# Optimization experiments

Hardware: AMD Instinct MI355X
Metric: run time of the kernel (lower is better)

## Reference

```python
import jax, jax.numpy as jnp
import numpy as np

DIM = 512
HEADS = 8
DHEAD = 64
INNER = HEADS * DHEAD
CHUNK = 8
GAMMA = 1.0
EPS = 1e-8
LN_EPS = 1e-5


def setup_inputs() -> dict:
    key = jax.random.key(0)
    ks = jax.random.split(key, 10)
    B, N = 64, 256
    return {
        "q": jax.random.normal(ks[0], (B, N, DIM), jnp.float32),
        "k": jax.random.normal(ks[1], (B, N, DIM), jnp.float32),
        "v": jax.random.normal(ks[2], (B, N, DIM), jnp.float32),
        "ln_gamma": jnp.ones((DIM,), jnp.float32),
        "ln_beta": jnp.zeros((DIM,), jnp.float32),
        "W_in": jax.random.normal(ks[3], (DIM, INNER), jnp.float32) / np.sqrt(DIM),
        "W_out": jax.random.normal(ks[4], (INNER, DIM), jnp.float32) / np.sqrt(INNER),
        "b_out": jnp.zeros((DIM,), jnp.float32),
        "cov_logit": jnp.asarray(0.6, jnp.float32),
        "var_logit": jnp.asarray(0.2, jnp.float32),
        "use_advanced": 1,
    }


def _layernorm(x, g, b):
    mu = jnp.mean(x, axis=-1, keepdims=True)
    var = jnp.mean(jnp.square(x - mu), axis=-1, keepdims=True)
    return (x - mu) * jax.lax.rsqrt(var + LN_EPS) * g + b


def _transform(t, ln_gamma, ln_beta, W_in):
    # [B,N,dim] -> [h,B,N,d]
    B, N, _ = t.shape
    f = _layernorm(t, ln_gamma, ln_beta) @ W_in
    return f.reshape(B, N, HEADS, DHEAD).transpose(2, 0, 1, 3)


def _chunk_stats(E):
    # E: [M, N, d], chunks of size CHUNK over M. Returns per-chunk scalars V, C of shape [M//CHUNK].
    M, N, d = E.shape
    nc = M // CHUNK
    Ec = E.reshape(nc, CHUNK, N, d)
    # variance component: torch.var is unbiased (ddof=1) over seq dim
    sigma = jnp.sqrt(jnp.var(Ec, axis=2, ddof=1) + EPS)  # [nc, CHUNK, d]
    V = jnp.mean(jax.nn.relu(GAMMA - sigma), axis=(1, 2))  # [nc]
    # covariance component: per-sample off-diagonal energy, averaged per chunk
    centered = Ec - jnp.mean(Ec, axis=2, keepdims=True)
    cov = jnp.einsum("csni,csnj->csij", centered, centered) / (N - 1)  # [nc,CHUNK,d,d]
    total = jnp.sum(jnp.square(cov), axis=(2, 3))
    diag = jnp.sum(jnp.square(jnp.diagonal(cov, axis1=2, axis2=3)), axis=2)
    C = jnp.mean((total - diag) / d, axis=1)  # [nc]
    return V, C


def reference(q, k, v, ln_gamma, ln_beta, W_in, W_out, b_out, cov_logit, var_logit, use_advanced):
    f_q = _transform(q, ln_gamma, ln_beta, W_in)  # [h,B,N,d]
    f_k = _transform(k, ln_gamma, ln_beta, W_in)
    f_v = _transform(v, ln_gamma, ln_beta, W_in)
    h, B, N, d = f_q.shape

    # cosine similarity
    dots_qk = jnp.einsum("hbnd,hbmd->hbnm", f_q, f_k)
    qn = jnp.linalg.norm(f_q, axis=-1)  # [h,B,N]
    kn = jnp.linalg.norm(f_k, axis=-1)
    cosine_sim = dots_qk / (qn[..., :, None] * kn[..., None, :])

    if use_advanced:
        Vq, Cq = _chunk_stats(f_q.reshape(h * B, N, d))
        Vk, Ck = _chunk_stats(f_k.reshape(h * B, N, d))
        var_component = jnp.repeat(Vq * Vk, CHUNK).reshape(h, B, 1, 1)
        cov_component = jnp.repeat(Cq * Ck, CHUNK).reshape(h, B, 1, 1)
    else:
        qc = f_q - jnp.mean(f_q, axis=-1, keepdims=True)
        kc = f_k - jnp.mean(f_k, axis=-1, keepdims=True)
        cov_component = jnp.einsum("hbnd,hbmd->hbnm", qc, kc) / d
        q_var = jnp.var(f_q, axis=-1, ddof=1, keepdims=True)  # [h,B,N,1]
        k_var = jnp.var(f_k, axis=-1, ddof=1, keepdims=True)
        var_component = (q_var * jnp.swapaxes(k_var, -1, -2)) / d

    cov_w = jax.nn.sigmoid(cov_logit)
    var_w = jax.nn.sigmoid(var_logit)
    cos_w = 1.0 - cov_w - var_w
    dots = cos_w * cosine_sim + cov_w * cov_component + var_w * var_component
    out = jnp.einsum("hbnm,hbmd->hbnd", dots, f_v)
    out = out.transpose(1, 2, 0, 3).reshape(B, N, h * d)
    return out @ W_out + b_out
```

## Files before the change

### kernel.cpp

```cpp
#include <hip/hip_runtime.h>
#include <cstdint>
#include <cstddef>

#define DIM    512
#define HEADS  8
#define DHEAD  64
#define NSEQ   256
#define BATCH  64
#define NROWS  (BATCH * NSEQ)
#define HB     (HEADS * BATCH)

typedef unsigned short u16;
typedef __bf16 bf16x8 __attribute__((ext_vector_type(8)));
typedef float  f32x4  __attribute__((ext_vector_type(4)));

__device__ __forceinline__ float sigmoidf_(float x) { return 1.0f / (1.0f + expf(-x)); }

__device__ __forceinline__ u16 f2bf(float f) {
    union { float f; unsigned u; } a; a.f = f;
    return (u16)((a.u + 0x7fffu + ((a.u >> 16) & 1u)) >> 16);
}

__device__ __forceinline__ void gload16(const void* g, void* l) {
    __builtin_amdgcn_global_load_lds((const __attribute__((address_space(1))) void*)g,
                                     (__attribute__((address_space(3))) void*)l, 16, 0, 0);
}

__global__ __launch_bounds__(256)
void transpose_cast_kernel(const float* __restrict__ W0, const float* __restrict__ W1,
                           u16* __restrict__ WT)
{
    __shared__ float tile[64][65];
    const int t = threadIdx.x;
    const int bx = blockIdx.x * 64, by = blockIdx.y * 64;
    const float* W = blockIdx.z ? W1 : W0;
    u16* dst = WT + (size_t)blockIdx.z * 512 * 512;
#pragma unroll
    for (int i = 0; i < 16; ++i) {
        int idx = i * 256 + t, r = idx >> 6, c = idx & 63;
        tile[r][c] = W[(size_t)(by + r) * DIM + bx + c];
    }
    __syncthreads();
#pragma unroll
    for (int i = 0; i < 16; ++i) {
        int idx = i * 256 + t, r = idx >> 6, c = idx & 63;
        dst[(size_t)(bx + r) * DIM + by + c] = f2bf(tile[c][r]);
    }
}

__global__ __launch_bounds__(256)
void ln_cast_kernel(const float* __restrict__ qp, const float* __restrict__ kp,
                    const float* __restrict__ vp, const float* __restrict__ gam,
                    const float* __restrict__ bet, u16* __restrict__ out)
{
    const int wid = threadIdx.x >> 6, lane = threadIdx.x & 63;
    const int row = blockIdx.x * 4 + wid;
    const int tns = row >> 14, lr = row & 16383;
    const float* X = (tns == 0) ? qp : (tns == 1) ? kp : vp;
    const float* xr = X + (size_t)lr * DIM;
    float4 a = *(const float4*)(xr + lane * 8);
    float4 b = *(const float4*)(xr + lane * 8 + 4);
    float v[8] = {a.x, a.y, a.z, a.w, b.x, b.y, b.z, b.w};
    float s = 0.f;
#pragma unroll
    for (int i = 0; i < 8; ++i) s += v[i];
#pragma unroll
    for (int o = 32; o > 0; o >>= 1) s += __shfl_xor(s, o, 64);
    const float mu = s * (1.f / DIM);
    float sq = 0.f;
#pragma unroll
    for (int i = 0; i < 8; ++i) { float d = v[i] - mu; sq += d * d; }
#pragma unroll
    for (int o = 32; o > 0; o >>= 1) sq += __shfl_xor(sq, o, 64);
    const float rstd = rsqrtf(sq * (1.f / DIM) + 1e-5f);
    float4 g0 = *(const float4*)(gam + lane * 8), g1 = *(const float4*)(gam + lane * 8 + 4);
    float4 b0 = *(const float4*)(bet + lane * 8), b1 = *(const float4*)(bet + lane * 8 + 4);
    float gv[8] = {g0.x, g0.y, g0.z, g0.w, g1.x, g1.y, g1.z, g1.w};
    float bv[8] = {b0.x, b0.y, b0.z, b0.w, b1.x, b1.y, b1.z, b1.w};
    union { u16 h[8]; uint4 u; } o16;
#pragma unroll
    for (int i = 0; i < 8; ++i) o16.h[i] = f2bf((v[i] - mu) * rstd * gv[i] + bv[i]);
    *(uint4*)(out + (size_t)row * DIM + lane * 8) = o16.u;
}

__global__ __launch_bounds__(256)
void in_gemm_kernel(const u16* __restrict__ A, const u16* __restrict__ BT,
                    u16* __restrict__ FT, u16* __restrict__ Fseq)
{
    __shared__ u16 shm[128 * 136];
    u16* Ct = shm;
    const int t = threadIdx.x, lane = t & 63, w = t >> 6;
    const int wr = w >> 1, wc = w & 1;
    const int flat = blockIdx.y * 4 + blockIdx.x;
    const int rt = (flat & 7) * 48 + ((flat >> 3) >> 2);
    const int c0 = ((flat >> 3) & 3) * 128;
    const int r0 = rt * 128;
    const int cl = lane & 15, q = lane >> 4;

    f32x4 acc[4][4];
#pragma unroll
    for (int i = 0; i < 4; ++i)
#pragma unroll
        for (int j = 0; j < 4; ++j) acc[i][j] = (f32x4){0.f, 0.f, 0.f, 0.f};

#define STAGE_IN(buf, kk)                                                        \
    {                                                                            \
        _Pragma("unroll")                                                        \
        for (int i = 0; i < 2; ++i) {                                            \
            int idx = i * 256 + t;                                               \
            int row = idx >> 2, ch = idx & 3;                                    \
            gload16(A  + (size_t)(r0 + row) * DIM + (kk) + ch * 8,               \
                    shm + (buf) * 4096 + idx * 8);                               \
            gload16(BT + (size_t)(c0 + row) * DIM + (kk) + ch * 8,               \
                    shm + 8192 + (buf) * 4096 + idx * 8);                        \
        }                                                                        \
    }

#define COMPUTE_IN(buf)                                                          \
    {                                                                            \
        const u16* As = shm + (buf) * 4096;                                      \
        const u16* Bs = shm + 8192 + (buf) * 4096;                               \
        bf16x8 af[4], bfr[4];                                                    \
        _Pragma("unroll")                                                        \
        for (int mi = 0; mi < 4; ++mi)                                           \
            af[mi] = *(const bf16x8*)(As + (wr * 64 + mi * 16 + cl) * 32 + q * 8); \
        _Pragma("unroll")                                                        \
        for (int ni = 0; ni < 4; ++ni)                                           \
            bfr[ni] = *(const bf16x8*)(Bs + (wc * 64 + ni * 16 + cl) * 32 + q * 8); \
        _Pragma("unroll")                                                        \
        for (int mi = 0; mi < 4; ++mi)                                           \
            _Pragma("unroll")                                                    \
            for (int ni = 0; ni < 4; ++ni)                                       \
                acc[mi][ni] = __builtin_amdgcn_mfma_f32_16x16x32_bf16(af[mi],    \
                                  bfr[ni], acc[mi][ni], 0, 0, 0);                \
    }

    STAGE_IN(0, 0);
    __syncthreads();
    for (int k0 = 0; k0 < DIM; k0 += 64) {
        STAGE_IN(1, k0 + 32);
        COMPUTE_IN(0);
        __syncthreads();
        if (k0 + 64 < DIM) STAGE_IN(0, k0 + 64);
        COMPUTE_IN(1);
        __syncthreads();
    }
#undef STAGE_IN
#undef COMPUTE_IN

    const int tns = r0 >> 14, b = (r0 >> 8) & 63, n0 = r0 & 255;
    const int lr0 = r0 & 16383;

    if (tns == 0) {
#pragma unroll
        for (int mi = 0; mi < 4; ++mi) {
            int lrow = wr * 64 + mi * 16 + q * 4;
#pragma unroll
            for (int ni = 0; ni < 4; ++ni) {
                int lcol = wc * 64 + ni * 16 + cl;
#pragma unroll
                for (int r = 0; r < 4; ++r)
                    Ct[(lrow + r) * 136 + lcol] = f2bf(acc[mi][ni][r]);
            }
        }
        __syncthreads();
#pragma unroll
        for (int i = 0; i < 8; ++i) {
            int idx = t + 256 * i, row = idx >> 4, ch = idx & 15;
            *(uint4*)(Fseq + (size_t)(lr0 + row) * DIM + c0 + ch * 8) =
                *(const uint4*)(Ct + row * 136 + ch * 8);
        }
        __syncthreads();
    }
#pragma unroll
    for (int mi = 0; mi < 4; ++mi) {
        int lrow = wr * 64 + mi * 16 + q * 4;
#pragma unroll
        for (int ni = 0; ni < 4; ++ni) {
            int lcol = wc * 64 + ni * 16 + cl;
#pragma unroll
            for (int r = 0; r < 4; ++r)
                Ct[lcol * 136 + lrow + r] = f2bf(acc[mi][ni][r]);
        }
    }
    __syncthreads();
#pragma unroll
    for (int i = 0; i < 8; ++i) {
        int idx = t + 256 * i, lc = idx >> 4, ch = idx & 15;
        *(uint4*)(FT + (((size_t)(tns * 64 + b) * 512 + c0 + lc) * 256 + n0 + ch * 8)) =
            *(const uint4*)(Ct + lc * 136 + ch * 8);
    }
}

__global__ __launch_bounds__(256)
void stats_kernel(const u16* __restrict__ FT, float* __restrict__ norms,
                  float2* __restrict__ vc)
{
    __shared__ u16 ET[64 * 264];
    __shared__ float mu[64];
    __shared__ float red[4][64];
    __shared__ float wr3[4][3];
    const int hb = blockIdx.x, tns = blockIdx.y, h = hb >> 6, b = hb & 63;
    const int t = threadIdx.x, lane = t & 63, w = t >> 6, cl = lane & 15, q = lane >> 4;
    const size_t Fb = ((size_t)(tns * 64 + b) * 512 + h * 64) * 256;

#pragma unroll
    for (int i = 0; i < 8; ++i) {
        int idx = t + 256 * i;
        int row = idx >> 5, ch = idx & 31;
        *(bf16x8*)(ET + row * 264 + ch * 8) =
            *(const bf16x8*)(FT + Fb + (size_t)row * 256 + ch * 8);
    }
    __syncthreads();

    {
        float s = 0.f;
#pragma unroll
        for (int d = 0; d < 64; ++d) {
            float x = (float)*(const __bf16*)(ET + d * 264 + t);
            s += x * x;
        }
        norms[((size_t)tns * HB + hb) * 256 + t] = sqrtf(s);
    }
    {
        int d = t & 63, part = t >> 6;
        float s = 0.f;
#pragma unroll
        for (int i = 0; i < 8; ++i) {
            bf16x8 v8 = *(const bf16x8*)(ET + d * 264 + part * 64 + i * 8);
#pragma unroll
            for (int j = 0; j < 8; ++j) s += (float)v8[j];
        }
        red[part][d] = s;
    }
    __syncthreads();
    if (t < 64) mu[t] = (red[0][t] + red[1][t] + red[2][t] + red[3][t]) * (1.f / 256.f);
    __syncthreads();

    f32x4 g[4];
#pragma unroll
    for (int nj = 0; nj < 4; ++nj) g[nj] = (f32x4){0.f, 0.f, 0.f, 0.f};
#pragma unroll
    for (int ks = 0; ks < 8; ++ks) {
        bf16x8 af = *(const bf16x8*)(ET + (16 * w + cl) * 264 + ks * 32 + q * 8);
#pragma unroll
        for (int nj = 0; nj < 4; ++nj) {
            bf16x8 bfr = *(const bf16x8*)(ET + (16 * nj + cl) * 264 + ks * 32 + q * 8);
            g[nj] = __builtin_amdgcn_mfma_f32_16x16x32_bf16(af, bfr, g[nj], 0, 0, 0);
        }
    }
    float t2 = 0.f, d2 = 0.f, vs = 0.f;
#pragma unroll
    for (int nj = 0; nj < 4; ++nj) {
        int j = 16 * nj + cl;
        float mj = mu[j];
#pragma unroll
        for (int r = 0; r < 4; ++r) {
            int i = 16 * w + 4 * q + r;
            float gc = (g[nj][r] - 256.f * mu[i] * mj) * (1.f / 255.f);
            float g2 = gc * gc;
            t2 += g2;
            if (i == j) {
                d2 += g2;
                float sig = sqrtf(gc + 1e-8f);
                vs += fmaxf(1.f - sig, 0.f);
            }
        }
    }
#pragma unroll
    for (int o = 32; o > 0; o >>= 1) {
        t2 += __shfl_xor(t2, o, 64);
        d2 += __shfl_xor(d2, o, 64);
        vs += __shfl_xor(vs, o, 64);
    }
    if (lane == 0) { wr3[w][0] = t2; wr3[w][1] = d2; wr3[w][2] = vs; }
    __syncthreads();
    if (t == 0) {
        float T = 0.f, D = 0.f, V = 0.f;
        for (int i = 0; i < 4; ++i) { T += wr3[i][0]; D += wr3[i][1]; V += wr3[i][2]; }
        vc[(size_t)tns * HB + hb] = make_float2(V * (1.f / 64.f), (T - D) * (1.f / 64.f));
    }
}

__global__ __launch_bounds__(256)
void attn_kernel(const u16* __restrict__ FT, const u16* __restrict__ Fseq,
                 const float* __restrict__ norms, const float2* __restrict__ vc,
                 const float* __restrict__ cov_logit, const float* __restrict__ var_logit,
                 u16* __restrict__ G)
{
    __shared__ u16 pool[64 * 136 * 2];
    __shared__ float invq[256], invk[256], sv[64];
    const int hb = blockIdx.x & 511, h2 = blockIdx.x >> 9;
    const int h = hb >> 6, b = hb & 63;
    const int t = threadIdx.x, lane = t & 63, w = t >> 6, cl = lane & 15, q = lane >> 4;
    u16* KT = pool;
    u16* VT = pool + 64 * 136;
    u16* MT = pool;
    u16* Os = pool + 4608;

    const float cw = sigmoidf_(*cov_logit), vw = sigmoidf_(*var_logit);
    const float cosw = 1.f - cw - vw;
    float s_hb;
    {
        int basec = hb & ~7;
        float vq = 0, cq = 0, vk = 0, ck = 0;
#pragma unroll
        for (int m = 0; m < 8; ++m) {
            float2 a = vc[basec + m];       vq += a.x; cq += a.y;
            float2 bb = vc[HB + basec + m]; vk += bb.x; ck += bb.y;
        }
        s_hb = (cw * cq * ck + vw * vq * vk) * (1.f / 64.f);
    }

    invq[t] = 1.f / norms[((size_t)0 * HB + hb) * 256 + t];
    invk[t] = 1.f / norms[((size_t)1 * HB + hb) * 256 + t];
    __syncthreads();

    const size_t FTk = ((size_t)(1 * 64 + b) * 512 + h * 64) * 256;
    const size_t FTv = ((size_t)(2 * 64 + b) * 512 + h * 64) * 256;
    f32x4 acc1[4];
#pragma unroll
    for (int nj = 0; nj < 4; ++nj) acc1[nj] = (f32x4){0.f, 0.f, 0.f, 0.f};
    float sp[4] = {0.f, 0.f, 0.f, 0.f};

    for (int c = 0; c < 2; ++c) {
#pragma unroll
        for (int i = 0; i < 4; ++i) {
            int idx = t + 256 * i;
            int row = idx >> 4, ch = idx & 15;
            int n0 = c * 128 + ch * 8;
            bf16x8 kv = *(const bf16x8*)(FT + FTk + (size_t)row * 256 + n0);
            bf16x8 vv = *(const bf16x8*)(FT + FTv + (size_t)row * 256 + n0);
            bf16x8 ksc;
#pragma unroll
            for (int j = 0; j < 8; ++j) ksc[j] = (__bf16)((float)kv[j] * invk[n0 + j]);
            *(bf16x8*)(KT + row * 136 + ch * 8) = ksc;
            *(bf16x8*)(VT + row * 136 + ch * 8) = vv;
        }
        __syncthreads();
#pragma unroll
        for (int ks = 0; ks < 4; ++ks) {
            bf16x8 af = *(const bf16x8*)(KT + (16 * w + cl) * 136 + ks * 32 + q * 8);
#pragma unroll
            for (int nj = 0; nj < 4; ++nj) {
                bf16x8 bfr = *(const bf16x8*)(VT + (16 * nj + cl) * 136 + ks * 32 + q * 8);
                if (w == 0) {
                    float s = 0.f;
#pragma unroll
                    for (int j = 0; j < 8; ++j) s += (float)bfr[j];
                    sp[nj] += s;
                }
                acc1[nj] = __builtin_amdgcn_mfma_f32_16x16x32_bf16(af, bfr, acc1[nj], 0, 0, 0);
            }
        }
        __syncthreads();
    }
    if (w == 0) {
#pragma unroll
        for (int nj = 0; nj < 4; ++nj) {
            float s = sp[nj];
            s += __shfl_xor(s, 16, 64);
            s += __shfl_xor(s, 32, 64);
            if (q == 0) sv[16 * nj + cl] = s;
        }
    }
#pragma unroll
    for (int nj = 0; nj < 4; ++nj)
#pragma unroll
        for (int r = 0; r < 4; ++r)
            MT[(16 * nj + cl) * 72 + 16 * w + 4 * q + r] = f2bf(acc1[nj][r]);
    __syncthreads();

    f32x4 acc2[2][4];
#pragma unroll
    for (int mi = 0; mi < 2; ++mi)
#pragma unroll
        for (int nj = 0; nj < 4; ++nj) acc2[mi][nj] = (f32x4){0.f, 0.f, 0.f, 0.f};
    const size_t Fq = (size_t)(b * 256 + h2 * 128) * DIM + h * 64;
#pragma unroll
    for (int ks2 = 0; ks2 < 2; ++ks2) {
        bf16x8 bfm[4];
#pragma unroll
        for (int nj = 0; nj < 4; ++nj)
            bfm[nj] = *(const bf16x8*)(MT + (16 * nj + cl) * 72 + ks2 * 32 + q * 8);
#pragma unroll
        for (int mi = 0; mi < 2; ++mi) {
            bf16x8 aq = *(const bf16x8*)(Fseq + Fq +
                         (size_t)(32 * w + 16 * mi + cl) * DIM + ks2 * 32 + q * 8);
#pragma unroll
            for (int nj = 0; nj < 4; ++nj)
                acc2[mi][nj] = __builtin_amdgcn_mfma_f32_16x16x32_bf16(aq, bfm[nj],
                                                                       acc2[mi][nj], 0, 0, 0);
        }
    }
    __syncthreads();
#pragma unroll
    for (int mi = 0; mi < 2; ++mi) {
        int nloc = 32 * w + 16 * mi + 4 * q;
#pragma unroll
        for (int nj = 0; nj < 4; ++nj) {
            int j = 16 * nj + cl;
            float svj = sv[j];
#pragma unroll
            for (int r = 0; r < 4; ++r) {
                float o = cosw * acc2[mi][nj][r] * invq[h2 * 128 + nloc + r] + s_hb * svj;
                Os[(nloc + r) * 72 + j] = f2bf(o);
            }
        }
    }
    __syncthreads();
#pragma unroll
    for (int i = 0; i < 4; ++i) {
        int cidx = t + 256 * i;
        int row = cidx >> 3, ch = cidx & 7;
        *(uint4*)(G + (size_t)(b * 256 + h2 * 128 + row) * DIM + h * 64 + ch * 8) =
            *(const uint4*)(Os + row * 72 + ch * 8);
    }
}

__global__ __launch_bounds__(256)
void out_gemm_kernel(const u16* __restrict__ A, const u16* __restrict__ BT,
                     const float* __restrict__ bias, float* __restrict__ C)
{
    __shared__ u16 shm[12288];
    const int t = threadIdx.x, lane = t & 63, w = t >> 6;
    const int wr = w >> 1, wc = w & 1;
    const int flat = blockIdx.y * 8 + blockIdx.x;
    const int rt = (flat & 7) * 16 + ((flat >> 3) >> 3);
    const int c0 = ((flat >> 3) & 7) * 64;
    const int r0 = rt * 128;
    const int cl = lane & 15, q = lane >> 4;

    f32x4 acc[4][2];
#pragma unroll
    for (int i = 0; i < 4; ++i)
#pragma unroll
        for (int j = 0; j < 2; ++j) acc[i][j] = (f32x4){0.f, 0.f, 0.f, 0.f};

#define STAGE_OUT(buf, kk)                                                       \
    {                                                                            \
        _Pragma("unroll")                                                        \
        for (int i = 0; i < 2; ++i) {                                            \
            int idx = i * 256 + t;                                               \
            int row = idx >> 2, ch = idx & 3;                                    \
            gload16(A + (size_t)(r0 + row) * DIM + (kk) + ch * 8,                \
                    shm + (buf) * 4096 + idx * 8);                               \
        }                                                                        \
        {                                                                        \
            int row = t >> 2, ch = t & 3;                                        \
            gload16(BT + (size_t)(c0 + row) * DIM + (kk) + ch * 8,               \
                    shm + 8192 + (buf) * 2048 + t * 8);                          \
        }                                                                        \
    }

#define COMPUTE_OUT(buf)                                                         \
    {                                                                            \
        const u16* As = shm + (buf) * 4096;                                      \
        const u16* Bs = shm + 8192 + (buf) * 2048;                               \
        bf16x8 af[4], bfr[2];                                                    \
        _Pragma("unroll")                                                        \
        for (int mi = 0; mi < 4; ++mi)                                           \
            af[mi] = *(const bf16x8*)(As + (wr * 64 + mi * 16 + cl) * 32 + q * 8); \
        _Pragma("unroll")                                                        \
        for (int ni = 0; ni < 2; ++ni)                                           \
            bfr[ni] = *(const bf16x8*)(Bs + (wc * 32 + ni * 16 + cl) * 32 + q * 8); \
        _Pragma("unroll")                                                        \
        for (int mi = 0; mi < 4; ++mi)                                           \
            _Pragma("unroll")                                                    \
            for (int ni = 0; ni < 2; ++ni)                                       \
                acc[mi][ni] = __builtin_amdgcn_mfma_f32_16x16x32_bf16(af[mi],    \
                                  bfr[ni], acc[mi][ni], 0, 0, 0);                \
    }

    STAGE_OUT(0, 0);
    __syncthreads();
    for (int k0 = 0; k0 < DIM; k0 += 64) {
        STAGE_OUT(1, k0 + 32);
        COMPUTE_OUT(0);
        __syncthreads();
        if (k0 + 64 < DIM) STAGE_OUT(0, k0 + 64);
        COMPUTE_OUT(1);
        __syncthreads();
    }
#undef STAGE_OUT
#undef COMPUTE_OUT

#pragma unroll
    for (int mi = 0; mi < 4; ++mi) {
        int row0 = r0 + wr * 64 + mi * 16 + q * 4;
#pragma unroll
        for (int ni = 0; ni < 2; ++ni) {
            int col = c0 + wc * 32 + ni * 16 + cl;
            float bv = bias[col];
#pragma unroll
            for (int r = 0; r < 4; ++r)
                C[(size_t)(row0 + r) * DIM + col] = acc[mi][ni][r] + bv;
        }
    }
}

extern "C" void kernel_launch(void* const* d_in, const int* in_sizes, int n_in,
                              void* d_out, int out_size, void* d_ws, size_t ws_size,
                              hipStream_t stream)
{
    const float* q         = (const float*)d_in[0];
    const float* k         = (const float*)d_in[1];
    const float* v         = (const float*)d_in[2];
    const float* ln_g      = (const float*)d_in[3];
    const float* ln_b      = (const float*)d_in[4];
    const float* W_in      = (const float*)d_in[5];
    const float* W_out     = (const float*)d_in[6];
    const float* b_out     = (const float*)d_in[7];
    const float* cov_logit = (const float*)d_in[8];
    const float* var_logit = (const float*)d_in[9];
    float* out = (float*)d_out;

    char* base = (char*)d_ws;
    u16*    Abf   = (u16*)base;
    u16*    WT    = (u16*)(base + 50331648);
    u16*    FT    = (u16*)(base + 51380224);
    u16*    Fseq  = (u16*)(base + 101711872);
    float*  norms = (float*)(base + 118489088);
    float2* vc    = (float2*)(base + 119537664);
    u16*    Gb    = Abf;

    transpose_cast_kernel<<<dim3(8, 8, 2), 256, 0, stream>>>(W_in, W_out, WT);
    ln_cast_kernel<<<dim3(3 * NROWS / 4), 256, 0, stream>>>(q, k, v, ln_g, ln_b, Abf);
    in_gemm_kernel<<<dim3(4, 3 * NROWS / 128), 256, 0, stream>>>(Abf, WT, FT, Fseq);
    stats_kernel<<<dim3(HB, 2), 256, 0, stream>>>(FT, norms, vc);
    attn_kernel<<<dim3(2 * HB), 256, 0, stream>>>(FT, Fseq, norms, vc,
                                                  cov_logit, var_logit, Gb);
    out_gemm_kernel<<<dim3(8, NROWS / 128), 256, 0, stream>>>(
        Gb, WT + 512 * 512, b_out, out);
}
```

Baseline: 245.2 us.

## Merge weight-transpose and layernorm kernels; skip redundant transposed Q writes

Combines the weight transpose/cast and layernorm/cast kernels into one launch that dispatches on block index, removing one kernel launch. The input GEMM now writes either the sequence-major or the transposed layout, not both. Which one depends on its branch condition, presumably q gets only Fseq. The stats kernel therefore reads q from Fseq and transposes it in shared memory with scalar 16-bit stores, which can cause LDS bank conflicts. This removes a full global write of the transposed q features.

```diff
diff --git a/kernel.cpp b/kernel.cpp
--- a/kernel.cpp
+++ b/kernel.cpp
@@ -27,60 +27,64 @@
 }
 
 __global__ __launch_bounds__(256)
-void transpose_cast_kernel(const float* __restrict__ W0, const float* __restrict__ W1,
-                           u16* __restrict__ WT)
+void prep_kernel(const float* __restrict__ qp, const float* __restrict__ kp,
+                 const float* __restrict__ vp, const float* __restrict__ gam,
+                 const float* __restrict__ bet, u16* __restrict__ out,
+                 const float* __restrict__ W0, const float* __restrict__ W1,
+                 u16* __restrict__ WT)
 {
     __shared__ float tile[64][65];
+    const int bid = blockIdx.x;
     const int t = threadIdx.x;
-    const int bx = blockIdx.x * 64, by = blockIdx.y * 64;
-    const float* W = blockIdx.z ? W1 : W0;
-    u16* dst = WT + (size_t)blockIdx.z * 512 * 512;
-#pragma unroll
-    for (int i = 0; i < 16; ++i) {
-        int idx = i * 256 + t, r = idx >> 6, c = idx & 63;
-        tile[r][c] = W[(size_t)(by + r) * DIM + bx + c];
-    }
-    __syncthreads();
-#pragma unroll
-    for (int i = 0; i < 16; ++i) {
-        int idx = i * 256 + t, r = idx >> 6, c = idx & 63;
-        dst[(size_t)(bx + r) * DIM + by + c] = f2bf(tile[c][r]);
-    }
-}
-
-__global__ __launch_bounds__(256)
-void ln_cast_kernel(const float* __restrict__ qp, const float* __restrict__ kp,
-                    const float* __restrict__ vp, const float* __restrict__ gam,
-                    const float* __restrict__ bet, u16* __restrict__ out)
-{
-    const int wid = threadIdx.x >> 6, lane = threadIdx.x & 63;
-    const int row = blockIdx.x * 4 + wid;
-    const int tns = row >> 14, lr = row & 16383;
-    const float* X = (tns == 0) ? qp : (tns == 1) ? kp : vp;
-    const float* xr = X + (size_t)lr * DIM;
-    float4 a = *(const float4*)(xr + lane * 8);
-    float4 b = *(const float4*)(xr + lane * 8 + 4);
-    float v[8] = {a.x, a.y, a.z, a.w, b.x, b.y, b.z, b.w};
-    float s = 0.f;
-#pragma unroll
-    for (int i = 0; i < 8; ++i) s += v[i];
-#pragma unroll
-    for (int o = 32; o > 0; o >>= 1) s += __shfl_xor(s, o, 64);
-    const float mu = s * (1.f / DIM);
-    float sq = 0.f;
-#pragma unroll
-    for (int i = 0; i < 8; ++i) { float d = v[i] - mu; sq += d * d; }
-#pragma unroll
-    for (int o = 32; o > 0; o >>= 1) sq += __shfl_xor(sq, o, 64);
-    const float rstd = rsqrtf(sq * (1.f / DIM) + 1e-5f);
-    float4 g0 = *(const float4*)(gam + lane * 8), g1 = *(const float4*)(gam + lane * 8 + 4);
-    float4 b0 = *(const float4*)(bet + lane * 8), b1 = *(const float4*)(bet + lane * 8 + 4);
-    float gv[8] = {g0.x, g0.y, g0.z, g0.w, g1.x, g1.y, g1.z, g1.w};
-    float bv[8] = {b0.x, b0.y, b0.z, b0.w, b1.x, b1.y, b1.z, b1.w};
-    union { u16 h[8]; uint4 u; } o16;
-#pragma unroll
-    for (int i = 0; i < 8; ++i) o16.h[i] = f2bf((v[i] - mu) * rstd * gv[i] + bv[i]);
-    *(uint4*)(out + (size_t)row * DIM + lane * 8) = o16.u;
+
+    if (bid < 12288) {
+        const int wid = t >> 6, lane = t & 63;
+        const int row = bid * 4 + wid;
+        const int tns = row >> 14, lr = row & 16383;
+        const float* X = (tns == 0) ? qp : (tns == 1) ? kp : vp;
+        const float* xr = X + (size_t)lr * DIM;
+        float4 a = *(const float4*)(xr + lane * 8);
+        float4 b = *(const float4*)(xr + lane * 8 + 4);
+        float v[8] = {a.x, a.y, a.z, a.w, b.x, b.y, b.z, b.w};
+        float s = 0.f;
+#pragma unroll
+        for (int i = 0; i < 8; ++i) s += v[i];
+#pragma unroll
+        for (int o = 32; o > 0; o >>= 1) s += __shfl_xor(s, o, 64);
+        const float mu = s * (1.f / DIM);
+        float sq = 0.f;
+#pragma unroll
+        for (int i = 0; i < 8; ++i) { float d = v[i] - mu; sq += d * d; }
+#pragma unroll
+        for (int o = 32; o > 0; o >>= 1) sq += __shfl_xor(sq, o, 64);
+        const float rstd = rsqrtf(sq * (1.f / DIM) + 1e-5f);
+        float4 g0 = *(const float4*)(gam + lane * 8), g1 = *(const float4*)(gam + lane * 8 + 4);
+        float4 b0 = *(const float4*)(bet + lane * 8), b1 = *(const float4*)(bet + lane * 8 + 4);
+        float gv[8] = {g0.x, g0.y, g0.z, g0.w, g1.x, g1.y, g1.z, g1.w};
+        float bv[8] = {b0.x, b0.y, b0.z, b0.w, b1.x, b1.y, b1.z, b1.w};
+        union { u16 h[8]; uint4 u; } o16;
+#pragma unroll
+        for (int i = 0; i < 8; ++i) o16.h[i] = f2bf((v[i] - mu) * rstd * gv[i] + bv[i]);
+        *(uint4*)(out + (size_t)row * DIM + lane * 8) = o16.u;
+    } else {
+        const int tid2 = bid - 12288;
+        const int z = tid2 >> 6;
+        const int rem = tid2 & 63;
+        const int by = (rem >> 3) * 64, bx = (rem & 7) * 64;
+        const float* W = z ? W1 : W0;
+        u16* dst = WT + (size_t)z * 512 * 512;
+#pragma unroll
+        for (int i = 0; i < 16; ++i) {
+            int idx = i * 256 + t, r = idx >> 6, c = idx & 63;
+            tile[r][c] = W[(size_t)(by + r) * DIM + bx + c];
+        }
+        __syncthreads();
+#pragma unroll
+        for (int i = 0; i < 16; ++i) {
+            int idx = i * 256 + t, r = idx >> 6, c = idx & 63;
+            dst[(size_t)(bx + r) * DIM + by + c] = f2bf(tile[c][r]);
+        }
+    }
 }
 
 __global__ __launch_bounds__(256)
@@ -170,31 +174,31 @@
             *(uint4*)(Fseq + (size_t)(lr0 + row) * DIM + c0 + ch * 8) =
                 *(const uint4*)(Ct + row * 136 + ch * 8);
         }
-        __syncthreads();
-    }
-#pragma unroll
-    for (int mi = 0; mi < 4; ++mi) {
-        int lrow = wr * 64 + mi * 16 + q * 4;
-#pragma unroll
-        for (int ni = 0; ni < 4; ++ni) {
-            int lcol = wc * 64 + ni * 16 + cl;
-#pragma unroll
-            for (int r = 0; r < 4; ++r)
-                Ct[lcol * 136 + lrow + r] = f2bf(acc[mi][ni][r]);
-        }
-    }
-    __syncthreads();
-#pragma unroll
-    for (int i = 0; i < 8; ++i) {
-        int idx = t + 256 * i, lc = idx >> 4, ch = idx & 15;
-        *(uint4*)(FT + (((size_t)(tns * 64 + b) * 512 + c0 + lc) * 256 + n0 + ch * 8)) =
-            *(const uint4*)(Ct + lc * 136 + ch * 8);
+    } else {
+#pragma unroll
+        for (int mi = 0; mi < 4; ++mi) {
+            int lrow = wr * 64 + mi * 16 + q * 4;
+#pragma unroll
+            for (int ni = 0; ni < 4; ++ni) {
+                int lcol = wc * 64 + ni * 16 + cl;
+#pragma unroll
+                for (int r = 0; r < 4; ++r)
+                    Ct[lcol * 136 + lrow + r] = f2bf(acc[mi][ni][r]);
+            }
+        }
+        __syncthreads();
+#pragma unroll
+        for (int i = 0; i < 8; ++i) {
+            int idx = t + 256 * i, lc = idx >> 4, ch = idx & 15;
+            *(uint4*)(FT + (((size_t)(tns * 64 + b) * 512 + c0 + lc) * 256 + n0 + ch * 8)) =
+                *(const uint4*)(Ct + lc * 136 + ch * 8);
+        }
     }
 }
 
 __global__ __launch_bounds__(256)
-void stats_kernel(const u16* __restrict__ FT, float* __restrict__ norms,
-                  float2* __restrict__ vc)
+void stats_kernel(const u16* __restrict__ FT, const u16* __restrict__ Fseq,
+                  float* __restrict__ norms, float2* __restrict__ vc)
 {
     __shared__ u16 ET[64 * 264];
     __shared__ float mu[64];
@@ -202,14 +206,27 @@
     __shared__ float wr3[4][3];
     const int hb = blockIdx.x, tns = blockIdx.y, h = hb >> 6, b = hb & 63;
     const int t = threadIdx.x, lane = t & 63, w = t >> 6, cl = lane & 15, q = lane >> 4;
-    const size_t Fb = ((size_t)(tns * 64 + b) * 512 + h * 64) * 256;
-
-#pragma unroll
-    for (int i = 0; i < 8; ++i) {
-        int idx = t + 256 * i;
-        int row = idx >> 5, ch = idx & 31;
-        *(bf16x8*)(ET + row * 264 + ch * 8) =
-            *(const bf16x8*)(FT + Fb + (size_t)row * 256 + ch * 8);
+
+    if (tns == 0) {
+#pragma unroll
+        for (int i = 0; i < 8; ++i) {
+            int idx = t + 256 * i;
+            int seqr = idx >> 3, ch = idx & 7;
+            union { bf16x8 v; u16 hh[8]; } u;
+            u.v = *(const bf16x8*)(Fseq + (size_t)(b * 256 + seqr) * 512 + h * 64 + ch * 8);
+#pragma unroll
+            for (int j = 0; j < 8; ++j)
+                ET[(ch * 8 + j) * 264 + seqr] = u.hh[j];
+        }
+    } else {
+        const size_t Fb = ((size_t)(1 * 64 + b) * 512 + h * 64) * 256;
+#pragma unroll
+        for (int i = 0; i < 8; ++i) {
+            int idx = t + 256 * i;
+            int row = idx >> 5, ch = idx & 31;
+            *(bf16x8*)(ET + row * 264 + ch * 8) =
+                *(const bf16x8*)(FT + Fb + (size_t)row * 256 + ch * 8);
+        }
     }
     __syncthreads();
 
@@ -524,10 +541,10 @@
     float2* vc    = (float2*)(base + 119537664);
     u16*    Gb    = Abf;
 
-    transpose_cast_kernel<<<dim3(8, 8, 2), 256, 0, stream>>>(W_in, W_out, WT);
-    ln_cast_kernel<<<dim3(3 * NROWS / 4), 256, 0, stream>>>(q, k, v, ln_g, ln_b, Abf);
+    prep_kernel<<<dim3(12288 + 128), 256, 0, stream>>>(q, k, v, ln_g, ln_b, Abf,
+                                                       W_in, W_out, WT);
     in_gemm_kernel<<<dim3(4, 3 * NROWS / 128), 256, 0, stream>>>(Abf, WT, FT, Fseq);
-    stats_kernel<<<dim3(HB, 2), 256, 0, stream>>>(FT, norms, vc);
+    stats_kernel<<<dim3(HB, 2), 256, 0, stream>>>(FT, Fseq, norms, vc);
     attn_kernel<<<dim3(2 * HB), 256, 0, stream>>>(FT, Fseq, norms, vc,
                                                   cov_logit, var_logit, Gb);
     out_gemm_kernel<<<dim3(8, NROWS / 128), 256, 0, stream>>>(
```

New measurement: 232.9 us. -5.0%, faster.
